# Kernel tuning notes

Hardware: AMD Instinct MI355X
Metric: run time of the kernel (lower is better)

## Reference

```python
import jax, jax.numpy as jnp
import numpy as np

BINS = jnp.array([1, 2, 3, 4, 8, 16, 32, 64], dtype=jnp.int32)
L = 10      # max span width
HID = 150   # Score hidden dim


def _mlp(x, W1, b1, W2, b2, W3, b3):
    # Score module: Linear -> ReLU -> Linear -> ReLU -> Linear (dropout = identity at eval)
    h = jax.nn.relu(x @ W1 + b1)
    h = jax.nn.relu(h @ W2 + b2)
    return h @ W3 + b3


def setup_inputs() -> dict:
    key = jax.random.key(0)
    ks = jax.random.split(key, 16)
    T, A, E, D, S = 8192, 1024, 512, 20, 32768
    GI = 2 * A + E + D  # 2580
    sc = lambda n: 1.0 / np.sqrt(n)
    return {
        "states": jax.random.normal(ks[0], (T, A), jnp.float32),
        "embeds": jax.random.normal(ks[1], (T, E), jnp.float32),
        "span_starts": jnp.sort(jax.random.randint(ks[2], (S,), 0, T - L)),
        "span_lengths": jax.random.randint(ks[3], (S,), 0, L),
        # attention Score params (attn_dim -> 150 -> 150 -> 1)
        "Wa1": jax.random.normal(ks[4], (A, HID), jnp.float32) * sc(A),
        "ba1": jnp.zeros((HID,), jnp.float32),
        "Wa2": jax.random.normal(ks[5], (HID, HID), jnp.float32) * sc(HID),
        "ba2": jnp.zeros((HID,), jnp.float32),
        "Wa3": jax.random.normal(ks[6], (HID, 1), jnp.float32) * sc(HID),
        "ba3": jnp.zeros((1,), jnp.float32),
        # Distance embedding table (len(bins)+1 = 9 buckets)
        "width_table": jax.random.normal(ks[7], (9, D), jnp.float32) * 0.1,
        # mention Score params (gi_dim -> 150 -> 150 -> 1)
        "Ws1": jax.random.normal(ks[8], (GI, HID), jnp.float32) * sc(GI),
        "bs1": jnp.zeros((HID,), jnp.float32),
        "Ws2": jax.random.normal(ks[9], (HID, HID), jnp.float32) * sc(HID),
        "bs2": jnp.zeros((HID,), jnp.float32),
        "Ws3": jax.random.normal(ks[10], (HID, 1), jnp.float32) * sc(HID),
        "bs3": jnp.zeros((1,), jnp.float32),
    }


def reference(states, embeds, span_starts, span_lengths,
              Wa1, ba1, Wa2, ba2, Wa3, ba3,
              width_table,
              Ws1, bs1, Ws2, bs2, Ws3, bs3):
    T = states.shape[0]
    # per-token attention logits: [T, 1]
    attns = _mlp(states, Wa1, ba1, Wa2, ba2, Wa3, ba3)

    pos = jnp.arange(L)
    idx = span_starts[:, None] + pos[None, :]                 # [S, L]
    mask = pos[None, :] <= span_lengths[:, None]              # valid positions
    idx = jnp.minimum(idx, T - 1)

    span_attn = jnp.where(mask, attns[idx, 0], -jnp.inf)      # [S, L]
    w = jax.nn.softmax(span_attn, axis=1)                     # per-span softmax
    pooled = jnp.einsum('sl,sle->se', w, embeds[idx])         # [S, E]

    ends = span_starts + span_lengths
    widths = span_lengths + 1
    bucket = jnp.searchsorted(BINS, widths.astype(jnp.int32), side='right')
    size_emb = width_table[bucket]                            # [S, D]

    g = jnp.concatenate([states[span_starts], states[ends], pooled, size_emb], axis=-1)
    scores = _mlp(g, Ws1, bs1, Ws2, bs2, Ws3, bs3)[:, 0]      # [S]
    return scores
```

## Files before the change

### kernel.cpp

```cpp
#include <hip/hip_runtime.h>
#include <math.h>

#define T_TOK 8192
#define A_DIM 1024
#define E_DIM 512
#define S_SPAN 32768
#define HID 150

typedef __attribute__((ext_vector_type(8))) short short8;
typedef __attribute__((ext_vector_type(4))) float f32x4;
typedef __attribute__((ext_vector_type(4))) unsigned int u32x4;

__device__ __forceinline__ unsigned short f2bf(float f) {
    unsigned int u = __builtin_bit_cast(unsigned int, f);
    u += 0x7FFFu + ((u >> 16) & 1u);
    return (unsigned short)(u >> 16);
}
__device__ __forceinline__ float bf2f(unsigned int h16) {
    unsigned int u = h16 << 16;
    return __builtin_bit_cast(float, u);
}
__device__ __forceinline__ short8 cast8(f32x4 a, f32x4 b) {
    short8 r;
    r[0] = (short)f2bf(a.x); r[1] = (short)f2bf(a.y);
    r[2] = (short)f2bf(a.z); r[3] = (short)f2bf(a.w);
    r[4] = (short)f2bf(b.x); r[5] = (short)f2bf(b.y);
    r[6] = (short)f2bf(b.z); r[7] = (short)f2bf(b.w);
    return r;
}

__device__ __forceinline__ void pub_barrier() {
    __builtin_amdgcn_sched_barrier(0);
    asm volatile("s_waitcnt lgkmcnt(0)" ::: "memory");
    __builtin_amdgcn_sched_barrier(0);
    __builtin_amdgcn_s_barrier();
    __builtin_amdgcn_sched_barrier(0);
}

struct WConv { const float* src; unsigned short* dst; int K0; int Kpad; int nblk; };
struct PrepTab {
    WConv g[6];
    const float* wt; const float* Ws1w; const float* bs1; float* PW;
    const float* castS; unsigned short* castSd;
    const float* castE; unsigned short* castEd;
};

__global__ __launch_bounds__(256) void prep_kernel(PrepTab tab) {
    __shared__ float tl[64][65];
    int b = blockIdx.x;
    #pragma unroll
    for (int gi = 0; gi < 6; ++gi) {
        if (b < tab.g[gi].nblk) {
            const int kt   = tab.g[gi].Kpad >> 6;
            const int j0   = (b / kt) * 64;
            const int k0   = (b % kt) * 64;
            const int K0   = tab.g[gi].K0;
            const int Kpad = tab.g[gi].Kpad;
            const int ty = threadIdx.x >> 6, tx = threadIdx.x & 63;
            const float* src = tab.g[gi].src;
            #pragma unroll
            for (int r = 0; r < 16; ++r) {
                int k = k0 + ty * 16 + r;
                int j = j0 + tx;
                tl[ty * 16 + r][tx] = (j < HID && k < K0)
                                      ? src[(size_t)k * HID + j] : 0.f;
            }
            __syncthreads();
            unsigned short* dst = tab.g[gi].dst;
            #pragma unroll
            for (int r = 0; r < 16; ++r) {
                int j = j0 + ty * 16 + r;
                if (j < 160)
                    dst[(size_t)j * Kpad + k0 + tx] = f2bf(tl[tx][ty * 16 + r]);
            }
            return;
        }
        b -= tab.g[gi].nblk;
    }
    if (b < 9) {
        int j = threadIdx.x;
        if (j < 160) {
            float acc = 0.f;
            if (j < HID) {
                for (int k = 0; k < 20; ++k)
                    acc = fmaf(tab.wt[b * 20 + k], tab.Ws1w[k * HID + j], acc);
                acc += tab.bs1[j];
            }
            tab.PW[b * 160 + j] = acc;
        }
        return;
    }
    b -= 9;
    const float* src; unsigned short* dst;
    size_t base;
    if (b < 4096) { src = tab.castS; dst = tab.castSd; base = (size_t)b * 2048; }
    else          { src = tab.castE; dst = tab.castEd; base = (size_t)(b - 4096) * 2048; }
    const size_t i = base + (size_t)threadIdx.x * 8;
    f32x4 f0 = *(const f32x4*)(src + i);
    f32x4 f1 = *(const f32x4*)(src + i + 4);
    *(short8*)(dst + i) = cast8(f0, f1);
}

struct GG {
    const void* A; int lda;
    const unsigned short* W; int K; int nrb;
    unsigned short* outh; int ldo;
    const float* bias; int relu;
    const float* dotv; const float* dotb; float* dotout;
    const unsigned short* W2; const float* bias2;
};
struct GTab { GG g[4]; int ng; };

template <int TAG>
__global__ __launch_bounds__(256) void gemm_fused(GTab tab) {
    constexpr int LDW = 72;
    __shared__ unsigned short WtL[2][160 * LDW];

    int b = blockIdx.x;
    int gi = 0;
    while (gi < tab.ng - 1 && b >= tab.g[gi].nrb) { b -= tab.g[gi].nrb; ++gi; }
    const GG G = tab.g[gi];

    const int tid = threadIdx.x;
    const int wid = tid >> 6;
    const int lane = tid & 63;
    const int l15 = lane & 15;
    const int quad = lane >> 4;
    const int row0 = b * 64 + wid * 16 + l15;
    const int K = G.K;
    const int nch = K >> 6;
    const unsigned short* Ah = (const unsigned short*)G.A + (size_t)row0 * G.lda;

    int sn[5], sk[5];
    #pragma unroll
    for (int i = 0; i < 5; ++i) { int u = tid + i * 256; sn[i] = u >> 3; sk[i] = (u & 7) * 8; }

    f32x4 acc[10];
    #pragma unroll
    for (int nt = 0; nt < 10; ++nt) acc[nt] = (f32x4){0.f, 0.f, 0.f, 0.f};

    u32x4 wA[5], wB[5];
    short8 hAa[2], hAb[2];
    short8 avc0, avc1;

#define LOAD_W(SET, KOFF)                                                     \
    {   _Pragma("unroll")                                                     \
        for (int i = 0; i < 5; ++i)                                           \
            SET[i] = *(const u32x4*)(G.W + (size_t)sn[i] * K + (KOFF) + sk[i]); }
#define LOAD_A(HSET, KOFF)                                                    \
    {   HSET[0] = *(const short8*)(Ah + (KOFF) + quad * 8);                   \
        HSET[1] = *(const short8*)(Ah + (KOFF) + 32 + quad * 8); }
#define STORE_W(SET, BUF)                                                     \
    {   _Pragma("unroll")                                                     \
        for (int i = 0; i < 5; ++i)                                           \
            *(u32x4*)&WtL[BUF][sn[i] * LDW + sk[i]] = SET[i]; }
#define SET_AVC(HSET)                                                         \
    {   avc0 = HSET[0]; avc1 = HSET[1]; }
#define MFMA_BLOCK(BUF)                                                       \
    {   _Pragma("unroll")                                                     \
        for (int nt = 0; nt < 10; ++nt) {                                     \
            short8 bv0 = *(const short8*)&WtL[BUF][(nt * 16 + l15) * LDW + quad * 8]; \
            acc[nt] = __builtin_amdgcn_mfma_f32_16x16x32_bf16(avc0, bv0, acc[nt], 0, 0, 0); \
            short8 bv1 = *(const short8*)&WtL[BUF][(nt * 16 + l15) * LDW + 32 + quad * 8]; \
            acc[nt] = __builtin_amdgcn_mfma_f32_16x16x32_bf16(avc1, bv1, acc[nt], 0, 0, 0); \
        } }

    LOAD_W(wA, 0);
    LOAD_A(hAa, 0);
    LOAD_W(wB, 64);
    LOAD_A(hAb, 64);
    STORE_W(wA, 0);
    SET_AVC(hAa);
    pub_barrier();

    for (int c = 0; c + 1 < nch; c += 2) {
        const bool mA = (c + 2 < nch);
        if (mA) {
            const int kn = (c + 2) << 6;
            LOAD_W(wA, kn);
            LOAD_A(hAa, kn);
        }
        STORE_W(wB, 1);
        MFMA_BLOCK(0);
        SET_AVC(hAb);
        pub_barrier();

        const bool mB = (c + 3 < nch);
        if (mB) {
            const int kn = (c + 3) << 6;
            LOAD_W(wB, kn);
            LOAD_A(hAb, kn);
        }
        if (mA) STORE_W(wA, 0);
        MFMA_BLOCK(1);
        if (mA) SET_AVC(hAa);
        pub_barrier();
    }
    if (nch & 1) {
        MFMA_BLOCK(0);
    }

#undef LOAD_W
#undef LOAD_A
#undef STORE_W
#undef SET_AVC
#undef MFMA_BLOCK

    const int rbase = b * 64 + wid * 16 + quad * 4;
    if (G.W2) {
        constexpr int LDH = 168;
        unsigned short* tile = &WtL[0][0] + wid * 16 * LDH;
        #pragma unroll
        for (int nt = 0; nt < 10; ++nt) {
            int col = nt * 16 + l15;
            float bv_ = (col < HID) ? G.bias[col] : 0.f;
            #pragma unroll
            for (int r = 0; r < 4; ++r) {
                float v = fmaxf(acc[nt][r] + bv_, 0.f);
                tile[(quad * 4 + r) * LDH + col] = f2bf(v);
            }
        }
        f32x4 acc2[10];
        #pragma unroll
        for (int nt = 0; nt < 10; ++nt) acc2[nt] = (f32x4){0.f, 0.f, 0.f, 0.f};
        #pragma unroll
        for (int kc = 0; kc < 5; ++kc) {
            short8 av = *(const short8*)&tile[l15 * LDH + kc * 32 + quad * 8];
            #pragma unroll
            for (int nt = 0; nt < 10; ++nt) {
                short8 bv = *(const short8*)(G.W2 + (size_t)(nt * 16 + l15) * 192 + kc * 32 + quad * 8);
                acc2[nt] = __builtin_amdgcn_mfma_f32_16x16x32_bf16(av, bv, acc2[nt], 0, 0, 0);
            }
        }
        float part[4] = {0.f, 0.f, 0.f, 0.f};
        #pragma unroll
        for (int nt = 0; nt < 10; ++nt) {
            int col = nt * 16 + l15;
            float b2 = (col < HID) ? G.bias2[col] : 0.f;
            float vv = (col < HID) ? G.dotv[col] : 0.f;
            #pragma unroll
            for (int r = 0; r < 4; ++r)
                part[r] += fmaxf(acc2[nt][r] + b2, 0.f) * vv;
        }
        #pragma unroll
        for (int r = 0; r < 4; ++r) {
            float p = part[r];
            #pragma unroll
            for (int off = 1; off < 16; off <<= 1) p += __shfl_xor(p, off);
            if (l15 == 0) G.dotout[rbase + r] = p + G.dotb[0];
        }
    } else if (G.dotout) {
        float part[4] = {0.f, 0.f, 0.f, 0.f};
        #pragma unroll
        for (int nt = 0; nt < 10; ++nt) {
            int col = nt * 16 + l15;
            float bv_ = (col < HID) ? G.bias[col] : 0.f;
            float vv = (col < HID) ? G.dotv[col] : 0.f;
            #pragma unroll
            for (int r = 0; r < 4; ++r)
                part[r] += fmaxf(acc[nt][r] + bv_, 0.f) * vv;
        }
        #pragma unroll
        for (int r = 0; r < 4; ++r) {
            float p = part[r];
            #pragma unroll
            for (int off = 1; off < 16; off <<= 1) p += __shfl_xor(p, off);
            if (l15 == 0) G.dotout[rbase + r] = p + G.dotb[0];
        }
    } else {
        #pragma unroll
        for (int nt = 0; nt < 10; ++nt) {
            int col = nt * 16 + l15;
            float bv_ = (G.bias != nullptr && col < HID) ? G.bias[col] : 0.f;
            #pragma unroll
            for (int r = 0; r < 4; ++r) {
                int row = rbase + r;
                float v = acc[nt][r] + bv_;
                if (G.relu) v = fmaxf(v, 0.f);
                G.outh[(size_t)row * G.ldo + col] = f2bf(v);
            }
        }
    }
}

__device__ __forceinline__ void add_bf8(f32x4& A, f32x4& B, u32x4 u) {
    A.x += bf2f(u.x & 0xffff); A.y += bf2f(u.x >> 16);
    A.z += bf2f(u.y & 0xffff); A.w += bf2f(u.y >> 16);
    B.x += bf2f(u.z & 0xffff); B.y += bf2f(u.z >> 16);
    B.z += bf2f(u.w & 0xffff); B.w += bf2f(u.w >> 16);
}
__device__ __forceinline__ void fma_bf8(f32x4& A, f32x4& B, u32x4 u, float w) {
    A.x = fmaf(w, bf2f(u.x & 0xffff), A.x); A.y = fmaf(w, bf2f(u.x >> 16), A.y);
    A.z = fmaf(w, bf2f(u.y & 0xffff), A.z); A.w = fmaf(w, bf2f(u.y >> 16), A.w);
    B.x = fmaf(w, bf2f(u.z & 0xffff), B.x); B.y = fmaf(w, bf2f(u.z >> 16), B.y);
    B.z = fmaf(w, bf2f(u.w & 0xffff), B.z); B.w = fmaf(w, bf2f(u.w >> 16), B.w);
}

__global__ __launch_bounds__(256) void span_l1_kernel(const float* __restrict__ attns,
                                                      const int* __restrict__ starts,
                                                      const int* __restrict__ lens,
                                                      const unsigned short* __restrict__ Ps,
                                                      const unsigned short* __restrict__ Pe,
                                                      const unsigned short* __restrict__ Pm,
                                                      const float* __restrict__ PW,
                                                      unsigned short* __restrict__ SH1) {
    const int wid = threadIdx.x >> 6;
    const int lane = threadIdx.x & 63;
    const int grp = lane >> 4;
    const int hl = lane & 15;
    const int gbase = lane & 48;
    const int s = blockIdx.x * 16 + wid * 4 + grp;
    const int start = starts[s];
    const int len = lens[s];

    const int iv = min(start + hl, T_TOK - 1);
    float a = (hl <= len) ? attns[iv] : -INFINITY;
    float m = a;
    #pragma unroll
    for (int off = 8; off; off >>= 1) m = fmaxf(m, __shfl_xor(m, off));
    float e = (hl <= len) ? __expf(a - m) : 0.f;
    float ssum = e;
    #pragma unroll
    for (int off = 8; off; off >>= 1) ssum += __shfl_xor(ssum, off);
    float wv = e / ssum;

    float wl[10]; int il[10];
    #pragma unroll
    for (int l = 0; l < 10; ++l) {
        wl[l] = __shfl(wv, gbase + l);
        il[l] = __shfl(iv, gbase + l) * 160;
    }

    const int end = start + len;
    const int width = len + 1;
    const int bucket = (width >= 1) + (width >= 2) + (width >= 3) + (width >= 4) +
                       (width >= 8) + (width >= 16) + (width >= 32) + (width >= 64);

    const unsigned short* ps = Ps + (size_t)start * 160;
    const unsigned short* pe = Pe + (size_t)end * 160;
    const float* pw = PW + bucket * 160;

    #pragma unroll
    for (int rep = 0; rep < 2; ++rep) {
        const int c = rep * 16 + hl;
        if (c < 20) {
            const int j0 = c * 8;
            f32x4 a0 = *(const f32x4*)(pw + j0);
            f32x4 a1 = *(const f32x4*)(pw + j0 + 4);
            add_bf8(a0, a1, *(const u32x4*)(ps + j0));
            add_bf8(a0, a1, *(const u32x4*)(pe + j0));
            #pragma unroll
            for (int l = 0; l < 10; ++l)
                fma_bf8(a0, a1, *(const u32x4*)(Pm + il[l] + j0), wl[l]);
            u32x4 pk;
            pk.x = (unsigned)f2bf(fmaxf(a0.x, 0.f)) | ((unsigned)f2bf(fmaxf(a0.y, 0.f)) << 16);
            pk.y = (unsigned)f2bf(fmaxf(a0.z, 0.f)) | ((unsigned)f2bf(fmaxf(a0.w, 0.f)) << 16);
            pk.z = (unsigned)f2bf(fmaxf(a1.x, 0.f)) | ((unsigned)f2bf(fmaxf(a1.y, 0.f)) << 16);
            pk.w = (unsigned)f2bf(fmaxf(a1.z, 0.f)) | ((unsigned)f2bf(fmaxf(a1.w, 0.f)) << 16);
            *(u32x4*)(SH1 + (size_t)s * 192 + j0) = pk;
        }
    }
}

extern "C" void kernel_launch(void* const* d_in, const int* in_sizes, int n_in,
                              void* d_out, int out_size, void* d_ws, size_t ws_size,
                              hipStream_t stream) {
    const float* states = (const float*)d_in[0];
    const float* embeds = (const float*)d_in[1];
    const int* span_starts = (const int*)d_in[2];
    const int* span_lengths = (const int*)d_in[3];
    const float* Wa1 = (const float*)d_in[4];
    const float* ba1 = (const float*)d_in[5];
    const float* Wa2 = (const float*)d_in[6];
    const float* ba2 = (const float*)d_in[7];
    const float* Wa3 = (const float*)d_in[8];
    const float* ba3 = (const float*)d_in[9];
    const float* width_table = (const float*)d_in[10];
    const float* Ws1 = (const float*)d_in[11];
    const float* bs1 = (const float*)d_in[12];
    const float* Ws2 = (const float*)d_in[13];
    const float* bs2 = (const float*)d_in[14];
    const float* Ws3 = (const float*)d_in[15];
    const float* bs3 = (const float*)d_in[16];
    float* out = (float*)d_out;

    char* w = (char*)d_ws;
    unsigned short* WtA  = (unsigned short*)w;  w += 480 * 1024 * 2;
    unsigned short* WtE  = (unsigned short*)w;  w += 160 * 512 * 2;
    unsigned short* Wa2t = (unsigned short*)w;  w += 160 * 192 * 2;
    unsigned short* Ws2t = (unsigned short*)w;  w += 160 * 192 * 2;
    float* PW    = (float*)w;                   w += 9 * 160 * 4;
    float* attns = (float*)w;                   w += 8192 * 4;
    unsigned short* Psh = (unsigned short*)w;   w += (size_t)T_TOK * 160 * 2;
    unsigned short* Peh = (unsigned short*)w;   w += (size_t)T_TOK * 160 * 2;
    unsigned short* Pmh = (unsigned short*)w;   w += (size_t)T_TOK * 160 * 2;
    unsigned short* SH1 = (unsigned short*)w;   w += (size_t)S_SPAN * 192 * 2;
    unsigned short* SB  = (unsigned short*)w;   w += (size_t)T_TOK * A_DIM * 2;
    unsigned short* EB  = (unsigned short*)w;   w += (size_t)T_TOK * E_DIM * 2;

    PrepTab pt;
    pt.g[0] = { Wa1,              WtA,              1024, 1024, 3 * (1024/64) };
    pt.g[1] = { Ws1,              WtA + 160*1024,   1024, 1024, 3 * (1024/64) };
    pt.g[2] = { Ws1 + 1024*150,   WtA + 320*1024,   1024, 1024, 3 * (1024/64) };
    pt.g[3] = { Ws1 + 2048*150,   WtE,               512,  512, 3 * (512/64)  };
    pt.g[4] = { Wa2,              Wa2t,              150,  192, 3 * (192/64)  };
    pt.g[5] = { Ws2,              Ws2t,              150,  192, 3 * (192/64)  };
    pt.wt = width_table; pt.Ws1w = Ws1 + 2560*150; pt.bs1 = bs1; pt.PW = PW;
    pt.castS = states; pt.castSd = SB;
    pt.castE = embeds; pt.castEd = EB;
    int wblk = 0; for (int i = 0; i < 6; ++i) wblk += pt.g[i].nblk;
    prep_kernel<<<wblk + 9 + 4096 + 2048, 256, 0, stream>>>(pt);

    GG z = {};

    GTab t1; t1.ng = 4;
    t1.g[0] = z; t1.g[0].A = SB; t1.g[0].lda = 1024; t1.g[0].W = WtA;            t1.g[0].K = 1024;
    t1.g[0].nrb = 128; t1.g[0].bias = ba1;
    t1.g[0].W2 = Wa2t; t1.g[0].bias2 = ba2;
    t1.g[0].dotv = Wa3; t1.g[0].dotb = ba3; t1.g[0].dotout = attns;
    t1.g[1] = z; t1.g[1].A = SB; t1.g[1].lda = 1024; t1.g[1].W = WtA + 160*1024; t1.g[1].K = 1024;
    t1.g[1].nrb = 128; t1.g[1].outh = Psh; t1.g[1].ldo = 160;
    t1.g[2] = z; t1.g[2].A = SB; t1.g[2].lda = 1024; t1.g[2].W = WtA + 320*1024; t1.g[2].K = 1024;
    t1.g[2].nrb = 128; t1.g[2].outh = Peh; t1.g[2].ldo = 160;
    t1.g[3] = z; t1.g[3].A = EB; t1.g[3].lda = 512;  t1.g[3].W = WtE;            t1.g[3].K = 512;
    t1.g[3].nrb = 128; t1.g[3].outh = Pmh; t1.g[3].ldo = 160;
    gemm_fused<1><<<512, 256, 0, stream>>>(t1);

    span_l1_kernel<<<S_SPAN / 16, 256, 0, stream>>>(attns, span_starts, span_lengths,
                                                    Psh, Peh, Pmh, PW, SH1);

    GTab t3; t3.ng = 1;
    t3.g[0] = z; t3.g[0].A = SH1; t3.g[0].lda = 192; t3.g[0].W = Ws2t; t3.g[0].K = 192;
    t3.g[0].nrb = 512; t3.g[0].bias = bs2; t3.g[0].dotv = Ws3; t3.g[0].dotb = bs3; t3.g[0].dotout = out;
    gemm_fused<3><<<512, 256, 0, stream>>>(t3);
}
```

Measured before the change: 166.9 us.

## Fuse span layer-1 gather with layer-2 MFMA and final dot

Merges the span gather/pool kernel with the second mention-MLP GEMM and the final dot product. Each block keeps its 16 spans' layer-1 activations in shared memory, runs the 150x150 layer with MFMA across four waves, and reduces the partial dot products through shared memory. This removes the SH1 round trip through global memory and one kernel launch. In exchange, each block re-reads the Ws2 weights from global or L2 memory, and each MFMA has only 16 rows.

```diff
diff --git a/kernel.cpp b/kernel.cpp
--- a/kernel.cpp
+++ b/kernel.cpp
@@ -249,24 +249,6 @@
             for (int off = 1; off < 16; off <<= 1) p += __shfl_xor(p, off);
             if (l15 == 0) G.dotout[rbase + r] = p + G.dotb[0];
         }
-    } else if (G.dotout) {
-        float part[4] = {0.f, 0.f, 0.f, 0.f};
-        #pragma unroll
-        for (int nt = 0; nt < 10; ++nt) {
-            int col = nt * 16 + l15;
-            float bv_ = (col < HID) ? G.bias[col] : 0.f;
-            float vv = (col < HID) ? G.dotv[col] : 0.f;
-            #pragma unroll
-            for (int r = 0; r < 4; ++r)
-                part[r] += fmaxf(acc[nt][r] + bv_, 0.f) * vv;
-        }
-        #pragma unroll
-        for (int r = 0; r < 4; ++r) {
-            float p = part[r];
-            #pragma unroll
-            for (int off = 1; off < 16; off <<= 1) p += __shfl_xor(p, off);
-            if (l15 == 0) G.dotout[rbase + r] = p + G.dotb[0];
-        }
     } else {
         #pragma unroll
         for (int nt = 0; nt < 10; ++nt) {
@@ -296,20 +278,30 @@
     B.z = fmaf(w, bf2f(u.w & 0xffff), B.z); B.w = fmaf(w, bf2f(u.w >> 16), B.w);
 }
 
-__global__ __launch_bounds__(256) void span_l1_kernel(const float* __restrict__ attns,
-                                                      const int* __restrict__ starts,
-                                                      const int* __restrict__ lens,
-                                                      const unsigned short* __restrict__ Ps,
-                                                      const unsigned short* __restrict__ Pe,
-                                                      const unsigned short* __restrict__ Pm,
-                                                      const float* __restrict__ PW,
-                                                      unsigned short* __restrict__ SH1) {
+__global__ __launch_bounds__(256) void span_all_kernel(
+        const float* __restrict__ attns,
+        const int* __restrict__ starts,
+        const int* __restrict__ lens,
+        const unsigned short* __restrict__ Ps,
+        const unsigned short* __restrict__ Pe,
+        const unsigned short* __restrict__ Pm,
+        const float* __restrict__ PW,
+        const unsigned short* __restrict__ W2,
+        const float* __restrict__ bs2,
+        const float* __restrict__ Ws3,
+        const float* __restrict__ bs3,
+        float* __restrict__ out) {
+    constexpr int LDH = 168;
+    __shared__ unsigned short tile[16 * LDH];
+    __shared__ float partials[4][16];
+
     const int wid = threadIdx.x >> 6;
     const int lane = threadIdx.x & 63;
     const int grp = lane >> 4;
     const int hl = lane & 15;
     const int gbase = lane & 48;
-    const int s = blockIdx.x * 16 + wid * 4 + grp;
+    const int sp = wid * 4 + grp;
+    const int s = blockIdx.x * 16 + sp;
     const int start = starts[s];
     const int len = lens[s];
 
@@ -357,8 +349,52 @@
             pk.y = (unsigned)f2bf(fmaxf(a0.z, 0.f)) | ((unsigned)f2bf(fmaxf(a0.w, 0.f)) << 16);
             pk.z = (unsigned)f2bf(fmaxf(a1.x, 0.f)) | ((unsigned)f2bf(fmaxf(a1.y, 0.f)) << 16);
             pk.w = (unsigned)f2bf(fmaxf(a1.z, 0.f)) | ((unsigned)f2bf(fmaxf(a1.w, 0.f)) << 16);
-            *(u32x4*)(SH1 + (size_t)s * 192 + j0) = pk;
-        }
+            *(u32x4*)&tile[sp * LDH + j0] = pk;
+        }
+    }
+    __syncthreads();
+
+    f32x4 acc[3];
+    #pragma unroll
+    for (int t = 0; t < 3; ++t) acc[t] = (f32x4){0.f, 0.f, 0.f, 0.f};
+    #pragma unroll
+    for (int kc = 0; kc < 5; ++kc) {
+        short8 av = *(const short8*)&tile[hl * LDH + kc * 32 + grp * 8];
+        #pragma unroll
+        for (int t = 0; t < 3; ++t) {
+            const int nt = wid + 4 * t;
+            if (nt < 10) {
+                short8 bv = *(const short8*)(W2 + (size_t)(nt * 16 + hl) * 192 + kc * 32 + grp * 8);
+                acc[t] = __builtin_amdgcn_mfma_f32_16x16x32_bf16(av, bv, acc[t], 0, 0, 0);
+            }
+        }
+    }
+
+    float part[4] = {0.f, 0.f, 0.f, 0.f};
+    #pragma unroll
+    for (int t = 0; t < 3; ++t) {
+        const int nt = wid + 4 * t;
+        if (nt < 10) {
+            int col = nt * 16 + hl;
+            float b2 = (col < HID) ? bs2[col] : 0.f;
+            float vv = (col < HID) ? Ws3[col] : 0.f;
+            #pragma unroll
+            for (int r = 0; r < 4; ++r)
+                part[r] += fmaxf(acc[t][r] + b2, 0.f) * vv;
+        }
+    }
+    #pragma unroll
+    for (int r = 0; r < 4; ++r) {
+        float p = part[r];
+        #pragma unroll
+        for (int off = 1; off < 16; off <<= 1) p += __shfl_xor(p, off);
+        if (hl == 0) partials[wid][grp * 4 + r] = p;
+    }
+    __syncthreads();
+    if (threadIdx.x < 16) {
+        float v = partials[0][threadIdx.x] + partials[1][threadIdx.x] +
+                  partials[2][threadIdx.x] + partials[3][threadIdx.x] + bs3[0];
+        out[blockIdx.x * 16 + threadIdx.x] = v;
     }
 }
 
@@ -394,7 +430,6 @@
     unsigned short* Psh = (unsigned short*)w;   w += (size_t)T_TOK * 160 * 2;
     unsigned short* Peh = (unsigned short*)w;   w += (size_t)T_TOK * 160 * 2;
     unsigned short* Pmh = (unsigned short*)w;   w += (size_t)T_TOK * 160 * 2;
-    unsigned short* SH1 = (unsigned short*)w;   w += (size_t)S_SPAN * 192 * 2;
     unsigned short* SB  = (unsigned short*)w;   w += (size_t)T_TOK * A_DIM * 2;
     unsigned short* EB  = (unsigned short*)w;   w += (size_t)T_TOK * E_DIM * 2;
 
@@ -426,11 +461,7 @@
     t1.g[3].nrb = 128; t1.g[3].outh = Pmh; t1.g[3].ldo = 160;
     gemm_fused<1><<<512, 256, 0, stream>>>(t1);
 
-    span_l1_kernel<<<S_SPAN / 16, 256, 0, stream>>>(attns, span_starts, span_lengths,
-                                                    Psh, Peh, Pmh, PW, SH1);
-
-    GTab t3; t3.ng = 1;
-    t3.g[0] = z; t3.g[0].A = SH1; t3.g[0].lda = 192; t3.g[0].W = Ws2t; t3.g[0].K = 192;
-    t3.g[0].nrb = 512; t3.g[0].bias = bs2; t3.g[0].dotv = Ws3; t3.g[0].dotb = bs3; t3.g[0].dotout = out;
-    gemm_fused<3><<<512, 256, 0, stream>>>(t3);
-}
+    span_all_kernel<<<S_SPAN / 16, 256, 0, stream>>>(attns, span_starts, span_lengths,
+                                                     Psh, Peh, Pmh, PW, Ws2t,
+                                                     bs2, Ws3, bs3, out);
+}
```

Measured after the change: 171.6 us. +2.8%, slower.
